# Optimization experiments

Hardware: AMD Instinct MI355X
Metric: run time of the kernel (lower is better)

The kernel has to match this reference:

```python
import jax, jax.numpy as jnp
import numpy as np
import math
from jax import lax


def _conv(x, w, b, stride=1, pad=0, groups=1):
    # x: [B,C,H,W], w: [O, C//groups, kh, kw] (OIHW)
    out = lax.conv_general_dilated(x, w, (stride, stride), [(pad, pad), (pad, pad)],
                                   feature_group_count=groups,
                                   dimension_numbers=('NCHW', 'OIHW', 'NCHW'))
    return out + b.reshape(1, -1, 1, 1)


def _shared_conv(x, k2d, b, stride=1, pad=0):
    # SharedConv: one [k,k] kernel shared across all channels (depthwise), scalar bias
    C = x.shape[1]
    w = jnp.broadcast_to(k2d[None, None], (C, 1) + k2d.shape)
    out = lax.conv_general_dilated(x, w, (stride, stride), [(pad, pad), (pad, pad)],
                                   feature_group_count=C,
                                   dimension_numbers=('NCHW', 'OIHW', 'NCHW'))
    return out + b


def _bn(x, g, b, m, v, eps=1e-5):
    scale = (g / jnp.sqrt(v + eps)).reshape(1, -1, 1, 1)
    return (x - m.reshape(1, -1, 1, 1)) * scale + b.reshape(1, -1, 1, 1)


def _leaky(x, s=0.01):
    return jnp.where(x >= 0, x, s * x)


def _max_leaky(x, t, s):
    # cap values above threshold with leaky slope
    return jnp.where(x <= t, x, t + s * (x - t))


def _min_leaky(x, t, s):
    # cap values below threshold with leaky slope
    return jnp.where(x >= t, x, t + s * (x - t))


def _mode_pool(x, k=11, padding=1):
    # histogram mode pooling: 17 bins over quantized values, stride 1
    xp = jnp.pad(x, ((0, 0), (0, 0), (padding, padding), (padding, padding)))
    bins = jnp.clip(jnp.round(xp * 16.0), 0.0, 16.0).astype(jnp.int32)
    oh = jax.nn.one_hot(bins, 17, dtype=x.dtype)           # [B,C,Hp,Wp,17]
    counts = lax.reduce_window(oh, 0.0, lax.add, (1, 1, k, k, 1), (1, 1, 1, 1, 1), 'VALID')
    return jnp.argmax(counts, axis=-1).astype(x.dtype) / 16.0


def _emphase(x, w, k=11):
    # EmphaseLocal: unsharp-style local emphasis with per-channel learnable scale
    s = lax.reduce_window(x, 0.0, lax.add, (1, 1, k, k), (1, 1, 1, 1), 'SAME')
    avg = s / float(k * k)
    return x + w.reshape(1, -1, 1, 1) * (x - avg)


def setup_inputs() -> dict:
    key = jax.random.key(0)
    ks = jax.random.split(key, 20)
    f32 = jnp.float32
    B, Cin, H, W = 2, 3, 512, 512
    C2 = 64  # half_out_channels * 2
    return {
        'x': jax.random.uniform(ks[0], (B, Cin, H, W), f32),
        'w1': jax.random.normal(ks[1], (C2, Cin, 1, 1), f32) * 0.1,
        'b1': jax.random.normal(ks[2], (C2,), f32) * 0.05,
        'w2': jax.random.normal(ks[3], (C2, 2, 1, 1), f32) * 0.1,  # groups=32
        'b2': jax.random.normal(ks[4], (C2,), f32) * 0.05,
        'down_k': jax.random.normal(ks[5], (3, 3), f32) * 0.1,
        'down_b': jax.random.normal(ks[6], (), f32) * 0.05,
        'ft_gamma': 1.0 + jax.random.normal(ks[7], (C2,), f32) * 0.1,
        'ft_beta': jax.random.normal(ks[8], (C2,), f32) * 0.05,
        'ft_mean': jax.random.normal(ks[9], (C2,), f32) * 0.05,
        'ft_var': jax.random.uniform(ks[10], (C2,), f32, 0.5, 1.5),
        'ft_k': jax.random.normal(ks[11], (1, 1), f32) * 0.5 + 1.0,
        'ft_b': jax.random.normal(ks[12], (), f32) * 0.05,
        'emph_w': jax.random.normal(ks[13], (C2,), f32) * 0.1,
        'interp_k': jax.random.normal(ks[14], (5, 5), f32) * 0.1,
        'interp_b': jax.random.normal(ks[15], (), f32) * 0.05,
        'i_gamma': 1.0 + jax.random.normal(ks[16], (C2,), f32) * 0.1,
        'i_beta': jax.random.normal(ks[17], (C2,), f32) * 0.05,
        'i_mean': jax.random.normal(ks[18], (C2,), f32) * 0.05,
        'i_var': jax.random.uniform(ks[19], (C2,), f32, 0.5, 1.5),
    }


def reference(x, w1, b1, w2, b2, down_k, down_b,
              ft_gamma, ft_beta, ft_mean, ft_var, ft_k, ft_b, emph_w,
              interp_k, interp_b, i_gamma, i_beta, i_mean, i_var):
    B, _, H, W = x.shape
    C2 = w1.shape[0]
    # prepare: ColorDownsample(16) -> ModePool2d(11,1,1) -> 1x1 conv -> MaxLeakyReLU -> grouped 1x1 conv -> MinLeakyReLU
    xd = jnp.round(x * 255.0 / 16.0) * 16.0 / 256.0
    h = _mode_pool(xd, k=11, padding=1)                 # [B,Cin,H-8,W-8]
    h = _max_leaky(_conv(h, w1, b1), 0.1, 0.01)
    groups = C2 // w2.shape[1]
    d = _min_leaky(_conv(h, w2, b2, groups=groups), 0.1, 0.01)
    score = jnp.zeros((B, C2, H, W), x.dtype)
    n = math.floor(math.log(min(d.shape[2], d.shape[3]), 3))
    for _ in range(n):
        # downgrade: shared 3x3 stride-3 conv + leaky
        d = _leaky(_shared_conv(d, down_k, down_b, stride=3, pad=1))
        # zoom back to full resolution, then interpolate branch (shared 5x5 conv + BN + leaky)
        z = jax.image.resize(d, (B, C2, H, W), method='bilinear')
        z = _bn(_shared_conv(z, interp_k, interp_b, pad=2), i_gamma, i_beta, i_mean, i_var)
        score = score + _leaky(z)
    # ft applied 3 times with shared weights: BN -> shared 1x1 conv -> EmphaseLocal
    for _ in range(3):
        s = _bn(score, ft_gamma, ft_beta, ft_mean, ft_var)
        s = _shared_conv(s, ft_k, ft_b)
        score = _emphase(s, emph_w, k=11)
    return score
```

## Files before the change

kernel.cpp:

```cpp
#include <hip/hip_runtime.h>

#define NB 2
#define CIN 3
#define HH 512
#define WW 512
#define C2 64
#define HM 504

typedef float v2f  __attribute__((ext_vector_type(2)));
typedef float v2fu __attribute__((ext_vector_type(2), aligned(4)));

__global__ __launch_bounds__(256) void k_mode(const float* __restrict__ x,
                                              unsigned char* __restrict__ hmode) {
  __shared__ unsigned char tile[26 * 26];
  int bc  = blockIdx.z;
  int ty0 = blockIdx.y * 16, tx0 = blockIdx.x * 16;
  const float* src = x + (size_t)bc * HH * WW;
  for (int i = threadIdx.x; i < 26 * 26; i += 256) {
    int r = i / 26, cl = i % 26;
    int Y = ty0 + r, X = tx0 + cl;
    unsigned char v = 0;
    if (Y >= 1 && Y <= HH && X >= 1 && X <= WW) {
      float val = src[(Y - 1) * WW + (X - 1)];
      float q = rintf((val * 255.0f) / 16.0f);
      q = fminf(fmaxf(q, 0.0f), 16.0f);
      v = (unsigned char)(int)q;
    }
    tile[i] = v;
  }
  __syncthreads();
  int ty = threadIdx.x >> 4, tx = threadIdx.x & 15;
  int oy = ty0 + ty, ox = tx0 + tx;
  if (oy >= HM || ox >= HM) return;
  unsigned long long w0 = 0, w1 = 0, w2 = 0;
  for (int dy = 0; dy < 11; dy++) {
    #pragma unroll
    for (int dx = 0; dx < 11; dx++) {
      int b = tile[(ty + dy) * 26 + tx + dx];
      unsigned long long inc = 1ull << ((b & 7) * 8);
      if (b < 8) w0 += inc;
      else if (b < 16) w1 += inc;
      else w2 += inc;
    }
  }
  int best = -1, bestb = 0;
  #pragma unroll
  for (int b = 0; b < 17; b++) {
    int cnt;
    if (b < 8)       cnt = (int)((w0 >> (b * 8)) & 0xff);
    else if (b < 16) cnt = (int)((w1 >> ((b - 8) * 8)) & 0xff);
    else             cnt = (int)(w2 & 0xff);
    if (cnt > best) { best = cnt; bestb = b; }
  }
  hmode[bc * HM * HM + oy * HM + ox] = (unsigned char)bestb;
}

__global__ __launch_bounds__(256) void k_prepare(const unsigned char* __restrict__ hmode,
                                                 const float* __restrict__ w1,
                                                 const float* __restrict__ b1,
                                                 const float* __restrict__ w2,
                                                 const float* __restrict__ b2,
                                                 const float* __restrict__ down_k,
                                                 const float* __restrict__ down_b,
                                                 float* __restrict__ d1) {
  int bc = blockIdx.y;
  int b  = bc >> 6;
  int c  = bc & 63;
  int pix = blockIdx.x * 256 + threadIdx.x;
  if (pix >= 168 * 168) return;
  int oy = pix / 168, ox = pix % 168;
  int c0 = (c >> 1) << 1;
  float w1a0 = w1[c0 * 3], w1a1 = w1[c0 * 3 + 1], w1a2 = w1[c0 * 3 + 2], b1a = b1[c0];
  float w1b0 = w1[(c0 + 1) * 3], w1b1 = w1[(c0 + 1) * 3 + 1], w1b2 = w1[(c0 + 1) * 3 + 2], b1b = b1[c0 + 1];
  float w2a = w2[c * 2], w2b = w2[c * 2 + 1], b2c = b2[c];
  float kb = *down_b;
  const unsigned char* h0p = hmode + (b * 3 + 0) * HM * HM;
  const unsigned char* h1p = hmode + (b * 3 + 1) * HM * HM;
  const unsigned char* h2p = hmode + (b * 3 + 2) * HM * HM;
  float acc = 0.0f;
  #pragma unroll
  for (int ky = 0; ky < 3; ky++) {
    int y = 3 * oy - 1 + ky;
    if (y < 0 || y >= HM) continue;
    #pragma unroll
    for (int kx = 0; kx < 3; kx++) {
      int xx = 3 * ox - 1 + kx;
      if (xx < 0 || xx >= HM) continue;
      int o = y * HM + xx;
      float hh0 = h0p[o] * (1.0f / 16.0f);
      float hh1 = h1p[o] * (1.0f / 16.0f);
      float hh2 = h2p[o] * (1.0f / 16.0f);
      float a0 = w1a0 * hh0 + w1a1 * hh1 + w1a2 * hh2 + b1a;
      float a1 = w1b0 * hh0 + w1b1 * hh1 + w1b2 * hh2 + b1b;
      a0 = (a0 <= 0.1f) ? a0 : 0.1f + 0.01f * (a0 - 0.1f);
      a1 = (a1 <= 0.1f) ? a1 : 0.1f + 0.01f * (a1 - 0.1f);
      float v = w2a * a0 + w2b * a1 + b2c;
      v = (v >= 0.1f) ? v : 0.1f + 0.01f * (v - 0.1f);
      acc += down_k[ky * 3 + kx] * v;
    }
  }
  float r = acc + kb;
  r = (r >= 0.0f) ? r : 0.01f * r;
  d1[bc * 168 * 168 + pix] = r;
}

__global__ __launch_bounds__(256) void k_down(const float* __restrict__ din,
                                              float* __restrict__ dout,
                                              const float* __restrict__ down_k,
                                              const float* __restrict__ down_b,
                                              int S, int So) {
  int bc = blockIdx.y;
  int pix = blockIdx.x * 256 + threadIdx.x;
  if (pix >= So * So) return;
  int oy = pix / So, ox = pix % So;
  const float* p = din + bc * S * S;
  float acc = 0.0f;
  #pragma unroll
  for (int ky = 0; ky < 3; ky++) {
    int y = 3 * oy - 1 + ky;
    if (y < 0 || y >= S) continue;
    #pragma unroll
    for (int kx = 0; kx < 3; kx++) {
      int xx = 3 * ox - 1 + kx;
      if (xx < 0 || xx >= S) continue;
      acc += down_k[ky * 3 + kx] * p[y * S + xx];
    }
  }
  float r = acc + *down_b;
  r = (r >= 0.0f) ? r : 0.01f * r;
  dout[bc * So * So + pix] = r;
}

__global__ __launch_bounds__(256) void k_lut(float2* __restrict__ lutpk) {
  int idx = blockIdx.x * 256 + threadIdx.x;
  if (idx >= 5 * 512) return;
  int lvl = idx >> 9, Y = idx & 511;
  const int Ls[5] = {168, 56, 19, 7, 3};
  int L = Ls[lvl];
  float f = (Y + 0.5f) * ((float)L / 512.0f) - 0.5f;
  f = fminf(fmaxf(f, 0.0f), (float)(L - 1));
  int y0 = (int)f;
  float w = f - (float)y0;
  lutpk[idx] = make_float2(__int_as_float(y0), w);
}

__global__ __launch_bounds__(256, 2) void k_score(const float* __restrict__ d1,
                                                  const float* __restrict__ d2,
                                                  const float* __restrict__ d3,
                                                  const float* __restrict__ d4,
                                                  const float* __restrict__ d5,
                                                  const float2* __restrict__ lutpk,
                                                  const float* __restrict__ interp_k,
                                                  const float* __restrict__ interp_b,
                                                  const float* __restrict__ i_gamma,
                                                  const float* __restrict__ i_beta,
                                                  const float* __restrict__ i_mean,
                                                  const float* __restrict__ i_var,
                                                  float* __restrict__ score) {
  __shared__ float z[68 * 68];
  __shared__ float rowIT[68 * 25];
  __shared__ float2 lyp[68];

  int bc = blockIdx.y;
  int c  = bc & 63;
  int tile = blockIdx.x;
  int tyi = tile >> 3, txi = tile & 7;
  int ty0 = tyi * 64, tx0 = txi * 64;
  bool interior = (tyi >= 1 && tyi <= 6 && txi >= 1 && txi <= 6);
  float K[25];
  #pragma unroll
  for (int i = 0; i < 25; i++)
    K[i] = __int_as_float(__builtin_amdgcn_readfirstlane(__float_as_int(interp_k[i])));
  float ib  = __int_as_float(__builtin_amdgcn_readfirstlane(__float_as_int(*interp_b)));
  float isc = i_gamma[c] * rsqrtf(i_var[c] + 1e-5f);
  float ibe = i_beta[c] - i_mean[c] * isc;
  int tid = threadIdx.x;
  int oyl = (tid >> 4) << 2, oxl = (tid & 15) << 2;
  float acc[4][4];
  #pragma unroll
  for (int i = 0; i < 4; i++)
    #pragma unroll
    for (int j = 0; j < 4; j++) acc[i][j] = 0.0f;

  const float* dls[5] = {d1, d2, d3, d4, d5};
  const int Ls[5]  = {168, 56, 19, 7, 3};
  const int RLs[5] = {24, 10, 5, 3, 3};

  auto phaseA = [&](int l) {
    int L = Ls[l], R = RLs[l];
    const float* dp = dls[l] + bc * L * L;
    const float2* lp = lutpk + (l << 9);
    int Ylo = max(ty0 - 2, 0);
    int r0 = __float_as_int(lp[Ylo].x);
    if (tid < 68) {
      int Yc = min(max(ty0 - 2 + tid, 0), 511);
      float2 pk = lp[Yc];
      lyp[tid] = make_float2(__int_as_float(__float_as_int(pk.x) - r0), pk.y);
    }
    for (int i = tid; i < R * 68; i += 256) {
      int r = i / 68, xx = i - r * 68;
      int Xc = min(max(tx0 - 2 + xx, 0), 511);
      float2 pk = lp[Xc];
      int ix = __float_as_int(pk.x);
      float wx = pk.y;
      int gr = min(r0 + r, L - 1);
      const float* rp = dp + gr * L + ix;
      float v0 = rp[0], v1 = rp[1];
      rowIT[xx * 25 + r] = v0 + wx * (v1 - v0);
    }
  };

  auto phaseB = [&]() {
    if (interior) {
      for (int i = tid; i < 68 * 68; i += 256) {
        int yy = i / 68, xx = i - yy * 68;
        float2 pk = lyp[yy];
        int a0 = __float_as_int(pk.x);
        const float* rp = &rowIT[xx * 25 + a0];
        float rA = rp[0], rB = rp[1];
        z[i] = rA + pk.y * (rB - rA);
      }
    } else {
      for (int i = tid; i < 68 * 68; i += 256) {
        int yy = i / 68, xx = i - yy * 68;
        float2 pk = lyp[yy];
        int a0 = __float_as_int(pk.x);
        const float* rp = &rowIT[xx * 25 + a0];
        float rA = rp[0], rB = rp[1];
        float v = rA + pk.y * (rB - rA);
        int Y = ty0 - 2 + yy, X = tx0 - 2 + xx;
        if (Y < 0 || Y >= 512 || X < 0 || X >= 512) v = 0.0f;
        z[i] = v;
      }
    }
  };

  auto convAcc = [&]() {
    v2f t2[4][2];
    #pragma unroll
    for (int i = 0; i < 4; i++) { t2[i][0] = (v2f)0.0f; t2[i][1] = (v2f)0.0f; }
    #pragma unroll
    for (int iy = 0; iy < 8; iy++) {
      const float4 za = *(const float4*)&z[(oyl + iy) * 68 + oxl];
      const float4 zb = *(const float4*)&z[(oyl + iy) * 68 + oxl + 4];
      v2f qq[7];
      qq[0].x = za.x; qq[0].y = za.y;
      qq[1].x = za.y; qq[1].y = za.z;
      qq[2].x = za.z; qq[2].y = za.w;
      qq[3].x = za.w; qq[3].y = zb.x;
      qq[4].x = zb.x; qq[4].y = zb.y;
      qq[5].x = zb.y; qq[5].y = zb.z;
      qq[6].x = zb.z; qq[6].y = zb.w;
      #pragma unroll
      for (int ky = 0; ky < 5; ky++) {
        const int o = iy - ky;
        if (o >= 0 && o < 4) {
          #pragma unroll
          for (int kx = 0; kx < 5; kx++) {
            float kv = K[ky * 5 + kx];
            v2f kk; kk.x = kv; kk.y = kv;
            t2[o][0] += kk * qq[kx];
            t2[o][1] += kk * qq[kx + 2];
          }
        }
      }
    }
    #pragma unroll
    for (int i = 0; i < 4; i++) {
      float tv[4] = {t2[i][0].x, t2[i][0].y, t2[i][1].x, t2[i][1].y};
      #pragma unroll
      for (int j = 0; j < 4; j++) {
        float v = (tv[j] + ib) * isc + ibe;
        v = (v >= 0.0f) ? v : 0.01f * v;
        acc[i][j] += v;
      }
    }
  };

  phaseA(0);
  __syncthreads();
  phaseB();
  #pragma unroll 1
  for (int l = 0; l < 5; l++) {
    __syncthreads();
    if (l < 4) phaseA(l + 1);
    convAcc();
    __syncthreads();
    if (l < 4) phaseB();
  }

  float* op = score + bc * 512 * 512;
  #pragma unroll
  for (int i = 0; i < 4; i++) {
    int Y = ty0 + oyl + i;
    float4 vv = make_float4(acc[i][0], acc[i][1], acc[i][2], acc[i][3]);
    *(float4*)(op + Y * 512 + tx0 + oxl) = vv;
  }
}

__global__ __launch_bounds__(256, 2) void k_ft_pipe(const float* __restrict__ s_in,
                                                    float* __restrict__ s_out,
                                                    const float* __restrict__ ft_gamma,
                                                    const float* __restrict__ ft_beta,
                                                    const float* __restrict__ ft_mean,
                                                    const float* __restrict__ ft_var,
                                                    const float* __restrict__ ft_k,
                                                    const float* __restrict__ ft_b,
                                                    const float* __restrict__ emph_w) {
  __shared__ float ring2[12 * 512];
  __shared__ float ring3[12 * 512];
  __shared__ float brow1[528];
  __shared__ float brow2[528];
  __shared__ float brow3[528];

  const int bc = blockIdx.y;
  const int c  = bc & 63;
  const int R0 = blockIdx.x << 7;
  const int mstart = R0 - 15;

  const float sc  = ft_gamma[c] * rsqrtf(ft_var[c] + 1e-5f);
  const float fk = *ft_k, fb = *ft_b;
  const float Aff = sc * fk;
  const float Cc  = (ft_beta[c] - ft_mean[c] * sc) * fk + fb;
  const float w   = emph_w[c];
  const float opw = 1.0f + w;
  const float okw = w * (1.0f / 121.0f);

  const int tid = threadIdx.x;
  const int x0  = tid << 1;

  const float* sp = s_in + ((size_t)bc << 18) + x0;
  float*       op = s_out + ((size_t)bc << 18) + x0;

  if (tid < 12) {
    int p = (tid < 6) ? tid : (512 + tid);
    brow1[p] = 0.0f; brow2[p] = 0.0f; brow3[p] = 0.0f;
  }

  auto ldraw = [&](int row) -> v2f {
    int rc = min(max(row, 0), 511);
    return *(const v2f*)(sp + ((size_t)rc << 9));
  };

  auto rowsum = [&](const float* b) -> v2f {
    const float* p = b + x0;
    v2f w0 = *(const v2f*)(p);
    v2f w1 = *(const v2f*)(p + 2);
    v2f w2 = *(const v2f*)(p + 4);
    v2f w3 = *(const v2f*)(p + 6);
    v2f w4 = *(const v2f*)(p + 8);
    v2f w5 = *(const v2f*)(p + 10);
    v2f w6 = *(const v2f*)(p + 12);
    float smid = ((w1.x + w1.y) + (w2.x + w2.y)) +
                 ((w3.x + w3.y) + (w4.x + w4.y)) + (w5.x + w5.y);
    v2f r;
    r.x = smid + w0.y;
    r.y = smid + w6.x;
    return r;
  };

  v2f cs1 = (v2f)0.0f, cs2 = (v2f)0.0f, cs3 = (v2f)0.0f;
  v2f out1p = (v2f)0.0f, out2p = (v2f)0.0f;

  int m = mstart;
  v2f gf = ldraw(m);
  v2f go = ldraw(m - 11);
  v2f gc = ldraw(m - 5);
  int sw = 0;

  #pragma unroll 1
  for (int i = 0; i < 160; ++i, ++m) {
    v2f gf_n = ldraw(m + 1);
    v2f go_n = ldraw(m - 10);
    v2f gc_n = ldraw(m - 4);

    int swn = (sw + 1 == 12) ? 0 : sw + 1;
    int swc = (sw + 7 >= 12) ? sw - 5 : sw + 7;

    {
      v2f u1f = (m >= 0 && m < 512) ? (gf * Aff + Cc) : (v2f)0.0f;
      int r = m - 11;
      v2f u1o = (r >= mstart && r >= 0 && r < 512) ? (go * Aff + Cc) : (v2f)0.0f;
      cs1 += u1f - u1o;
      *(v2f*)(brow1 + 6 + x0) = cs1;
    }
    {
      v2f u2s = out1p * Aff + Cc;
      *(v2f*)(ring2 + sw * 512 + x0) = u2s;
      int rf = m - 6;
      v2f u2f = (rf >= 0 && rf < 512) ? u2s : (v2f)0.0f;
      int r = m - 17;
      v2f u2or = *(const v2f*)(ring2 + swn * 512 + x0);
      v2f u2o = (r >= mstart - 6 && r >= 0 && r < 512) ? u2or : (v2f)0.0f;
      cs2 += u2f - u2o;
      *(v2f*)(brow2 + 6 + x0) = cs2;
    }
    {
      v2f u3s = out2p * Aff + Cc;
      *(v2f*)(ring3 + sw * 512 + x0) = u3s;
      int rf = m - 12;
      v2f u3f = (rf >= 0 && rf < 512) ? u3s : (v2f)0.0f;
      int r = m - 23;
      v2f u3or = *(const v2f*)(ring3 + swn * 512 + x0);
      v2f u3o = (r >= mstart - 12 && r >= 0 && r < 512) ? u3or : (v2f)0.0f;
      cs3 += u3f - u3o;
      *(v2f*)(brow3 + 6 + x0) = cs3;
    }
    __syncthreads();
    {
      int rc1 = m - 5;
      v2f u1c = (rc1 >= 0 && rc1 < 512) ? (gc * Aff + Cc) : (v2f)0.0f;
      v2f B1 = rowsum(brow1);
      out1p = u1c * opw - B1 * okw;
    }
    {
      int rc2 = m - 11;
      v2f u2cr = *(const v2f*)(ring2 + swc * 512 + x0);
      v2f u2c = (rc2 >= mstart - 6 && rc2 >= 0 && rc2 < 512) ? u2cr : (v2f)0.0f;
      v2f B2 = rowsum(brow2);
      out2p = u2c * opw - B2 * okw;
    }
    {
      int rc3 = m - 17;
      v2f u3cr = *(const v2f*)(ring3 + swc * 512 + x0);
      v2f u3c = (rc3 >= mstart - 12 && rc3 >= 0 && rc3 < 512) ? u3cr : (v2f)0.0f;
      v2f B3 = rowsum(brow3);
      v2f o3 = u3c * opw - B3 * okw;
      if (i >= 32)
        *(v2f*)(op + ((size_t)(m - 17) << 9)) = o3;
    }
    __syncthreads();
    gf = gf_n; go = go_n; gc = gc_n;
    sw = swn;
  }
}

extern "C" void kernel_launch(void* const* d_in, const int* in_sizes, int n_in,
                              void* d_out, int out_size, void* d_ws, size_t ws_size,
                              hipStream_t stream) {
  const float* x        = (const float*)d_in[0];
  const float* w1       = (const float*)d_in[1];
  const float* b1       = (const float*)d_in[2];
  const float* w2       = (const float*)d_in[3];
  const float* b2       = (const float*)d_in[4];
  const float* down_k   = (const float*)d_in[5];
  const float* down_b   = (const float*)d_in[6];
  const float* ft_gamma = (const float*)d_in[7];
  const float* ft_beta  = (const float*)d_in[8];
  const float* ft_mean  = (const float*)d_in[9];
  const float* ft_var   = (const float*)d_in[10];
  const float* ft_k     = (const float*)d_in[11];
  const float* ft_b     = (const float*)d_in[12];
  const float* emph_w   = (const float*)d_in[13];
  const float* interp_k = (const float*)d_in[14];
  const float* interp_b = (const float*)d_in[15];
  const float* i_gamma  = (const float*)d_in[16];
  const float* i_beta   = (const float*)d_in[17];
  const float* i_mean   = (const float*)d_in[18];
  const float* i_var    = (const float*)d_in[19];
  float* out = (float*)d_out;

  char* ws = (char*)d_ws;
  size_t off = 0;
  auto alloc = [&](size_t bytes) { size_t r = off; off += (bytes + 255) & ~(size_t)255; return r; };
  unsigned char* hmode = (unsigned char*)(ws + alloc((size_t)NB * CIN * HM * HM));
  float* d1 = (float*)(ws + alloc((size_t)NB * C2 * 168 * 168 * 4));
  float* d2 = (float*)(ws + alloc((size_t)NB * C2 * 56 * 56 * 4));
  float* d3 = (float*)(ws + alloc((size_t)NB * C2 * 19 * 19 * 4));
  float* d4 = (float*)(ws + alloc((size_t)NB * C2 * 7 * 7 * 4));
  float* d5 = (float*)(ws + alloc((size_t)NB * C2 * 3 * 3 * 4));
  float* s0 = (float*)(ws + alloc((size_t)NB * C2 * 512 * 512 * 4));
  float2* lutpk = (float2*)(ws + alloc((size_t)5 * 512 * 8));

  k_mode<<<dim3(32, 32, NB * CIN), 256, 0, stream>>>(x, hmode);
  k_lut<<<10, 256, 0, stream>>>(lutpk);
  k_prepare<<<dim3((168 * 168 + 255) / 256, NB * C2), 256, 0, stream>>>(
      hmode, w1, b1, w2, b2, down_k, down_b, d1);
  k_down<<<dim3((56 * 56 + 255) / 256, NB * C2), 256, 0, stream>>>(d1, d2, down_k, down_b, 168, 56);
  k_down<<<dim3((19 * 19 + 255) / 256, NB * C2), 256, 0, stream>>>(d2, d3, down_k, down_b, 56, 19);
  k_down<<<dim3((7 * 7 + 255) / 256, NB * C2), 256, 0, stream>>>(d3, d4, down_k, down_b, 19, 7);
  k_down<<<dim3((3 * 3 + 255) / 256, NB * C2), 256, 0, stream>>>(d4, d5, down_k, down_b, 7, 3);
  k_score<<<dim3(64, NB * C2), 256, 0, stream>>>(d1, d2, d3, d4, d5, lutpk,
                                                 interp_k, interp_b,
                                                 i_gamma, i_beta, i_mean, i_var, s0);
  k_ft_pipe<<<dim3(4, NB * C2), 256, 0, stream>>>(s0, out, ft_gamma, ft_beta, ft_mean,
                                                  ft_var, ft_k, ft_b, emph_w);
}
```

Measured before the change: 642.8 us.

## Fold vertical bilinear interpolation into per-row effective conv weights in k_score

The k_score kernel no longer builds the full 68x68 upsampled tile in shared memory. It keeps only the horizontally interpolated source rows. For each output row it precomputes folded coefficients that merge the vertical bilinear weights with the 5x5 kernel, so the conv reads at most 3-4 source rows instead of 8 upsampled rows. This removes the phaseB materialisation and cuts the shared-memory footprint, and the launch bounds are raised to 4 blocks per CU. In exchange it drops the prefetch overlap between levels, adds a serial per-level fill, and relies on each output row spanning at most 4 (level 0) or 3 source rows.

```diff
diff --git a/kernel.cpp b/kernel.cpp
--- a/kernel.cpp
+++ b/kernel.cpp
@@ -144,7 +144,7 @@
   lutpk[idx] = make_float2(__int_as_float(y0), w);
 }
 
-__global__ __launch_bounds__(256, 2) void k_score(const float* __restrict__ d1,
+__global__ __launch_bounds__(256, 4) void k_score(const float* __restrict__ d1,
                                                   const float* __restrict__ d2,
                                                   const float* __restrict__ d3,
                                                   const float* __restrict__ d4,
@@ -157,16 +157,15 @@
                                                   const float* __restrict__ i_mean,
                                                   const float* __restrict__ i_var,
                                                   float* __restrict__ score) {
-  __shared__ float z[68 * 68];
-  __shared__ float rowIT[68 * 25];
-  __shared__ float2 lyp[68];
+  __shared__ float xrow[24 * 68];
+  __shared__ float kap[64 * 4 * 8];
+  __shared__ int   abase[64];
 
   int bc = blockIdx.y;
   int c  = bc & 63;
   int tile = blockIdx.x;
   int tyi = tile >> 3, txi = tile & 7;
   int ty0 = tyi * 64, tx0 = txi * 64;
-  bool interior = (tyi >= 1 && tyi <= 6 && txi >= 1 && txi <= 6);
   float K[25];
   #pragma unroll
   for (int i = 0; i < 25; i++)
@@ -186,88 +185,75 @@
   const int Ls[5]  = {168, 56, 19, 7, 3};
   const int RLs[5] = {24, 10, 5, 3, 3};
 
-  auto phaseA = [&](int l) {
-    int L = Ls[l], R = RLs[l];
+  auto fillLevel = [&](int l) {
+    int L = Ls[l], RR = RLs[l];
     const float* dp = dls[l] + bc * L * L;
     const float2* lp = lutpk + (l << 9);
     int Ylo = max(ty0 - 2, 0);
     int r0 = __float_as_int(lp[Ylo].x);
-    if (tid < 68) {
-      int Yc = min(max(ty0 - 2 + tid, 0), 511);
-      float2 pk = lp[Yc];
-      lyp[tid] = make_float2(__int_as_float(__float_as_int(pk.x) - r0), pk.y);
-    }
-    for (int i = tid; i < R * 68; i += 256) {
-      int r = i / 68, xx = i - r * 68;
-      int Xc = min(max(tx0 - 2 + xx, 0), 511);
-      float2 pk = lp[Xc];
-      int ix = __float_as_int(pk.x);
-      float wx = pk.y;
-      int gr = min(r0 + r, L - 1);
-      const float* rp = dp + gr * L + ix;
-      float v0 = rp[0], v1 = rp[1];
-      rowIT[xx * 25 + r] = v0 + wx * (v1 - v0);
-    }
-  };
-
-  auto phaseB = [&]() {
-    if (interior) {
-      for (int i = tid; i < 68 * 68; i += 256) {
-        int yy = i / 68, xx = i - yy * 68;
-        float2 pk = lyp[yy];
-        int a0 = __float_as_int(pk.x);
-        const float* rp = &rowIT[xx * 25 + a0];
-        float rA = rp[0], rB = rp[1];
-        z[i] = rA + pk.y * (rB - rA);
-      }
-    } else {
-      for (int i = tid; i < 68 * 68; i += 256) {
-        int yy = i / 68, xx = i - yy * 68;
-        float2 pk = lyp[yy];
-        int a0 = __float_as_int(pk.x);
-        const float* rp = &rowIT[xx * 25 + a0];
-        float rA = rp[0], rB = rp[1];
-        float v = rA + pk.y * (rB - rA);
-        int Y = ty0 - 2 + yy, X = tx0 - 2 + xx;
-        if (Y < 0 || Y >= 512 || X < 0 || X >= 512) v = 0.0f;
-        z[i] = v;
-      }
-    }
-  };
-
-  auto convAcc = [&]() {
-    v2f t2[4][2];
-    #pragma unroll
-    for (int i = 0; i < 4; i++) { t2[i][0] = (v2f)0.0f; t2[i][1] = (v2f)0.0f; }
-    #pragma unroll
-    for (int iy = 0; iy < 8; iy++) {
-      const float4 za = *(const float4*)&z[(oyl + iy) * 68 + oxl];
-      const float4 zb = *(const float4*)&z[(oyl + iy) * 68 + oxl + 4];
-      v2f qq[7];
-      qq[0].x = za.x; qq[0].y = za.y;
-      qq[1].x = za.y; qq[1].y = za.z;
-      qq[2].x = za.z; qq[2].y = za.w;
-      qq[3].x = za.w; qq[3].y = zb.x;
-      qq[4].x = zb.x; qq[4].y = zb.y;
-      qq[5].x = zb.y; qq[5].y = zb.z;
-      qq[6].x = zb.z; qq[6].y = zb.w;
+    {
+      int y = tid >> 2, rr = tid & 3;
+      int Y = ty0 + y;
+      float kv0 = 0.0f, kv1 = 0.0f, kv2 = 0.0f, kv3 = 0.0f, kv4 = 0.0f;
+      int ab = -1;
       #pragma unroll
       for (int ky = 0; ky < 5; ky++) {
-        const int o = iy - ky;
-        if (o >= 0 && o < 4) {
-          #pragma unroll
-          for (int kx = 0; kx < 5; kx++) {
-            float kv = K[ky * 5 + kx];
-            v2f kk; kk.x = kv; kk.y = kv;
-            t2[o][0] += kk * qq[kx];
-            t2[o][1] += kk * qq[kx + 2];
-          }
+        int yy = Y + ky - 2;
+        if (yy >= 0 && yy < 512) {
+          float2 pk = lp[yy];
+          int a0 = __float_as_int(pk.x);
+          float wv = pk.y;
+          if (ab < 0) ab = a0;
+          float cf = 0.0f;
+          if (a0 - ab == rr)     cf += 1.0f - wv;
+          if (a0 + 1 - ab == rr) cf += wv;
+          kv0 += cf * K[ky * 5 + 0];
+          kv1 += cf * K[ky * 5 + 1];
+          kv2 += cf * K[ky * 5 + 2];
+          kv3 += cf * K[ky * 5 + 3];
+          kv4 += cf * K[ky * 5 + 4];
         }
       }
-    }
+      float* kp = &kap[tid << 3];
+      kp[0] = kv0; kp[1] = kv1; kp[2] = kv2; kp[3] = kv3; kp[4] = kv4;
+      if (rr == 0) abase[y] = ab - r0;
+    }
+    for (int i = tid; i < RR * 68; i += 256) {
+      int r = i / 68, xx = i - r * 68;
+      int X = tx0 - 2 + xx;
+      float v = 0.0f;
+      if (X >= 0 && X < 512) {
+        float2 pk = lp[X];
+        int ix = __float_as_int(pk.x);
+        float wx = pk.y;
+        int gr = min(r0 + r, L - 1);
+        const float* rp = dp + gr * L + ix;
+        float v0 = rp[0], v1 = rp[1];
+        v = v0 + wx * (v1 - v0);
+      }
+      xrow[r * 68 + xx] = v;
+    }
+  };
+
+  auto convAcc = [&](int rspan, int rlim) {
     #pragma unroll
     for (int i = 0; i < 4; i++) {
-      float tv[4] = {t2[i][0].x, t2[i][0].y, t2[i][1].x, t2[i][1].y};
+      int y = oyl + i;
+      int ab = abase[y];
+      float t0 = 0.0f, t1 = 0.0f, t2v = 0.0f, t3 = 0.0f;
+      for (int rr = 0; rr < rspan; rr++) {
+        int row = min(ab + rr, rlim);
+        const float* xp = &xrow[row * 68 + oxl];
+        float4 A = *(const float4*)xp;
+        float4 B = *(const float4*)(xp + 4);
+        const float* kp = &kap[(y << 5) + (rr << 3)];
+        float k0 = kp[0], k1 = kp[1], k2 = kp[2], k3 = kp[3], k4 = kp[4];
+        t0  += k0 * A.x + k1 * A.y + k2 * A.z + k3 * A.w + k4 * B.x;
+        t1  += k0 * A.y + k1 * A.z + k2 * A.w + k3 * B.x + k4 * B.y;
+        t2v += k0 * A.z + k1 * A.w + k2 * B.x + k3 * B.y + k4 * B.z;
+        t3  += k0 * A.w + k1 * B.x + k2 * B.y + k3 * B.z + k4 * B.w;
+      }
+      float tv[4] = {t0, t1, t2v, t3};
       #pragma unroll
       for (int j = 0; j < 4; j++) {
         float v = (tv[j] + ib) * isc + ibe;
@@ -277,16 +263,13 @@
     }
   };
 
-  phaseA(0);
-  __syncthreads();
-  phaseB();
   #pragma unroll 1
   for (int l = 0; l < 5; l++) {
+    if (l) __syncthreads();
+    fillLevel(l);
     __syncthreads();
-    if (l < 4) phaseA(l + 1);
-    convAcc();
-    __syncthreads();
-    if (l < 4) phaseB();
+    if (l == 0) convAcc(4, RLs[0] - 1);
+    else        convAcc(3, RLs[l] - 1);
   }
 
   float* op = score + bc * 512 * 512;
```

Result: faster. 582.3 us (-9.4%).
